# Optimization experiments

Measured on AMD Instinct MI355X. Metric: run time of the kernel, lower is better.

Reference implementation:

```python
import jax, jax.numpy as jnp
import numpy as np

E = 1024
M = 6
GH = 256
FR = 16  # FiLM bottleneck r = max(16, E//64)


def setup_inputs() -> dict:
    key = jax.random.key(0)
    ks = jax.random.split(key, 32)
    n = lambda k, shape, std=0.02: jax.random.normal(k, shape, dtype=jnp.float32) * std
    inp = {
        "x": jax.random.normal(ks[0], (4, 2048, E), dtype=jnp.float32),
        # gate MLP E->GH->M
        "gw1": n(ks[1], (E, GH)), "gb1": jnp.zeros((GH,), jnp.float32),
        "gw2": n(ks[2], (GH, M)), "gb2": jnp.zeros((M,), jnp.float32),
        "ebias": jnp.zeros((M,), jnp.float32),
        "pm_alpha": jnp.float32(0.5),
        # expert 0: DoubleMLP E->2E->E
        "dfc_w": n(ks[3], (E, 2 * E)), "dfc_b": jnp.zeros((2 * E,), jnp.float32),
        "dproj_w": n(ks[4], (2 * E, E)), "dproj_b": jnp.zeros((E,), jnp.float32),
        # expert 1: SingleMLP E->E->E
        "sfc_w": n(ks[5], (E, E)), "sfc_b": jnp.zeros((E,), jnp.float32),
        "sproj_w": n(ks[6], (E, E)), "sproj_b": jnp.zeros((E,), jnp.float32),
        # expert 2: rank-2 perceptron
        "p2_w": n(ks[7], (2, E)), "p2_v": n(ks[8], (2, E)),
        "p2_alpha": jnp.ones((2,), jnp.float32), "p2_b": jnp.zeros((2,), jnp.float32),
        "p2_bias": jnp.zeros((E,), jnp.float32),
        # expert 3: rank-4 perceptron
        "p4_w": n(ks[9], (4, E)), "p4_v": n(ks[10], (4, E)),
        "p4_alpha": jnp.ones((4,), jnp.float32), "p4_b": jnp.zeros((4,), jnp.float32),
        "p4_bias": jnp.zeros((E,), jnp.float32),
        # expert 4: ReGLU1D
        "rg_u": n(ks[11], (E,)), "rg_a": jnp.ones((E,), jnp.float32),
        "rg_b": jnp.zeros((1,), jnp.float32), "rg_bias": jnp.zeros((E,), jnp.float32),
        # expert 5: FiLM E->FR->2E
        "fl_dw": n(ks[12], (E, FR)), "fl_db": jnp.zeros((FR,), jnp.float32),
        "fl_uw": n(ks[13], (FR, 2 * E)), "fl_ub": jnp.zeros((2 * E,), jnp.float32),
    }
    return inp


def _gelu(x):
    return jax.nn.gelu(x, approximate=False)  # torch nn.GELU default (erf)


def _rank_n(x, w, v, alpha, b, biasvec):
    # y = biasvec + sum_i alpha_i * gelu(<w_i,x> + b_i) * v_i
    s = jnp.einsum("bse,ne->bsn", x, w) + b
    g = _gelu(s)
    return jnp.einsum("bsn,ne->bse", alpha * g, v) + biasvec


def reference(x, gw1, gb1, gw2, gb2, ebias, pm_alpha,
              dfc_w, dfc_b, dproj_w, dproj_b,
              sfc_w, sfc_b, sproj_w, sproj_b,
              p2_w, p2_v, p2_alpha, p2_b, p2_bias,
              p4_w, p4_v, p4_alpha, p4_b, p4_bias,
              rg_u, rg_a, rg_b, rg_bias,
              fl_dw, fl_db, fl_uw, fl_ub):
    # gate logits [B,S,M]; tau=1.0
    gl = _gelu(x @ gw1 + gb1) @ gw2 + gb2 + ebias
    pi = jax.nn.softmax(gl, axis=-1)
    # top_k=1 sparse weights: mask to top-1 then renormalize
    _, topi = jax.lax.top_k(pi, 1)
    mask = jax.nn.one_hot(topi[..., 0], M, dtype=pi.dtype)
    w = pi * mask
    w = w / (jnp.sum(w, axis=-1, keepdims=True) + 1e-9)

    # experts (dropout = identity in eval)
    o0 = _gelu(x @ dfc_w + dfc_b) @ dproj_w + dproj_b            # DoubleMLP
    o1 = _gelu(x @ sfc_w + sfc_b) @ sproj_w + sproj_b            # SingleMLP
    o2 = _rank_n(x, p2_w, p2_v, p2_alpha, p2_b, p2_bias)          # perc2
    o3 = _rank_n(x, p4_w, p4_v, p4_alpha, p4_b, p4_bias)          # perc4
    s = x @ rg_u + rg_b[0]                                        # ReGLU1D
    o4 = jax.nn.sigmoid(s)[..., None] * (x * rg_a) + rg_bias
    t = _gelu(x @ fl_dw + fl_db)                                  # FiLM
    gb = t @ fl_uw + fl_ub
    gamma, beta = jnp.split(gb, 2, axis=-1)
    o5 = gamma * x + beta

    all_out = jnp.stack([o0, o1, o2, o3, o4, o5], axis=-1)        # [B,S,E,M]
    mixed = jnp.sum(all_out * w[..., None, :], axis=-1)
    return pm_alpha * mixed
```

## Files before the change

### kernel.cpp

```cpp
#include <hip/hip_runtime.h>
#include <math.h>


#define E 1024
#define GH 256
#define NEXP 6
#define NTOK 8192
#define NCH 24

typedef __attribute__((ext_vector_type(8))) short bf16x8;
typedef __attribute__((ext_vector_type(4))) float f32x4;

__device__ __forceinline__ float gelu_erf(float v) {
    return 0.5f * v * (1.0f + erff(v * 0.70710678118654752440f));
}

__device__ __forceinline__ unsigned short f2bf(float f) {
    union { float f; unsigned u; } c; c.f = f;
    unsigned u = c.u;
    u += 0x7fffu + ((u >> 16) & 1u);
    return (unsigned short)(u >> 16);
}

__device__ __forceinline__ float bf2f(unsigned short h) {
    union { unsigned u; float f; } c; c.u = ((unsigned)h) << 16;
    return c.f;
}

__device__ __forceinline__ int ldso(int row, int q) {
    return row * 32 + ((q ^ ((row >> 1) & 3)) << 3);
}

__global__ __launch_bounds__(256)
void prep_kernel(const float* __restrict__ x, unsigned short* __restrict__ xh,
                 unsigned short* __restrict__ xl,
                 const float* __restrict__ gw1, unsigned short* __restrict__ w1cat,
                 const float* __restrict__ p2_w, const float* __restrict__ p4_w,
                 const float* __restrict__ rg_u, const float* __restrict__ fl_dw,
                 unsigned short* __restrict__ w1cheap,
                 const float* __restrict__ dfc_w, unsigned short* __restrict__ dfc_wt,
                 const float* __restrict__ dproj_w, unsigned short* __restrict__ dpj_wt,
                 const float* __restrict__ sfc_w, unsigned short* __restrict__ sfc_wt,
                 const float* __restrict__ sproj_w, unsigned short* __restrict__ spj_wt) {
    __shared__ float tile[32][33];
    const int tid = threadIdx.x;
    const int tx = tid & 31, ty = tid >> 5;
    int b = blockIdx.x;
    if (b < 2048) {
        const int n4 = NTOK * E / 4;
        for (int i = b * 256 + tid; i < n4; i += 2048 * 256) {
            float4 v = reinterpret_cast<const float4*>(x)[i];
            ushort4 h, l;
            h.x = f2bf(v.x); l.x = f2bf(v.x - bf2f(h.x));
            h.y = f2bf(v.y); l.y = f2bf(v.y - bf2f(h.y));
            h.z = f2bf(v.z); l.z = f2bf(v.z - bf2f(h.z));
            h.w = f2bf(v.w); l.w = f2bf(v.w - bf2f(h.w));
            reinterpret_cast<ushort4*>(xh)[i] = h;
            reinterpret_cast<ushort4*>(xl)[i] = l;
        }
        return;
    }
    b -= 2048;
    if (b < 256) {
        const int c0 = (b & 7) * 32, r0 = (b >> 3) * 32;
#pragma unroll
        for (int i = 0; i < 4; ++i)
            tile[ty + i * 8][tx] = gw1[(size_t)(r0 + ty + i * 8) * GH + c0 + tx];
        __syncthreads();
#pragma unroll
        for (int i = 0; i < 4; ++i) {
            float v = tile[tx][ty + i * 8];
            unsigned short h = f2bf(v);
            size_t row = (size_t)(c0 + ty + i * 8) * 2048;
            w1cat[row + r0 + tx] = h;
            w1cat[row + 1024 + r0 + tx] = f2bf(v - bf2f(h));
        }
        return;
    }
    b -= 256;
    if (b < 64) {
        const int r = b;
        const int k4 = tid * 4;
        float4 v = {0.f, 0.f, 0.f, 0.f};
        if (r < 2)       v = *reinterpret_cast<const float4*>(&p2_w[r * E + k4]);
        else if (r < 6)  v = *reinterpret_cast<const float4*>(&p4_w[(r - 2) * E + k4]);
        else if (r == 6) v = *reinterpret_cast<const float4*>(&rg_u[k4]);
        else if (r < 23) {
            const int j = r - 7;
            v.x = fl_dw[(k4 + 0) * 16 + j];
            v.y = fl_dw[(k4 + 1) * 16 + j];
            v.z = fl_dw[(k4 + 2) * 16 + j];
            v.w = fl_dw[(k4 + 3) * 16 + j];
        }
        ushort4 h, l;
        h.x = f2bf(v.x); l.x = f2bf(v.x - bf2f(h.x));
        h.y = f2bf(v.y); l.y = f2bf(v.y - bf2f(h.y));
        h.z = f2bf(v.z); l.z = f2bf(v.z - bf2f(h.z));
        h.w = f2bf(v.w); l.w = f2bf(v.w - bf2f(h.w));
        *reinterpret_cast<ushort4*>(&w1cheap[r * 2048 + k4]) = h;
        *reinterpret_cast<ushort4*>(&w1cheap[r * 2048 + 1024 + k4]) = l;
        return;
    }
    b -= 64;
    const float* src; unsigned short* dst; int R, C, nbx;
    if (b < 2048)      { src = dfc_w;   dst = dfc_wt; R = 1024; C = 2048; nbx = 64; }
    else if (b < 4096) { src = dproj_w; dst = dpj_wt; R = 2048; C = 1024; nbx = 32; b -= 2048; }
    else if (b < 5120) { src = sfc_w;   dst = sfc_wt; R = 1024; C = 1024; nbx = 32; b -= 4096; }
    else               { src = sproj_w; dst = spj_wt; R = 1024; C = 1024; nbx = 32; b -= 5120; }
    const int c0 = (b % nbx) * 32, r0 = (b / nbx) * 32;
#pragma unroll
    for (int i = 0; i < 4; ++i)
        tile[ty + i * 8][tx] = src[(size_t)(r0 + ty + i * 8) * C + c0 + tx];
    __syncthreads();
#pragma unroll
    for (int i = 0; i < 4; ++i)
        dst[(size_t)(c0 + ty + i * 8) * R + r0 + tx] = f2bf(tile[tx][ty + i * 8]);
}

__global__ __launch_bounds__(256)
void gate_partial_kernel(const unsigned short* __restrict__ xh,
                         const unsigned short* __restrict__ xl,
                         const unsigned short* __restrict__ w1cat,
                         const unsigned short* __restrict__ w1cheap,
                         float* __restrict__ hp0, float* __restrict__ hp1,
                         float* __restrict__ cdot0, float* __restrict__ cdot1) {
    __shared__ __align__(16) unsigned short As[2][64 * 32];
    __shared__ __align__(16) unsigned short Bs[2][64 * 32];
    const int tid = threadIdx.x;
    const int t0 = blockIdx.y * 64, n0 = blockIdx.x * 64, z = blockIdx.z;
    const unsigned short* A = z ? xl : xh;
    float* hp = z ? hp1 : hp0;
    float* cd = z ? cdot1 : cdot0;

    const int lane = tid & 63, wv = tid >> 6;
    const int wm = (wv & 1) * 32, wn = (wv >> 1) * 32;
    const int lm = lane & 15, q = lane >> 4;
    const int r0 = tid >> 2, gsl = tid & 3;
    const int g = gsl ^ ((r0 >> 1) & 3);
    const int so = r0 * 32 + gsl * 8;

    const unsigned short* pa = A + (size_t)(t0 + r0) * E + g * 8;
    const unsigned short* pb = w1cat + (size_t)(n0 + r0) * 2048 + g * 8;

    const bool docheap = (blockIdx.x == 0);
    const int tc = wv >> 1;
    const unsigned short* pcw = w1cheap + (size_t)(tc * 16 + lm) * 2048 + q * 8;

    f32x4 acc[2][2];
#pragma unroll
    for (int s = 0; s < 2; ++s)
#pragma unroll
        for (int t = 0; t < 2; ++t) acc[s][t] = (f32x4){0.f, 0.f, 0.f, 0.f};
    f32x4 accC[2];
    accC[0] = (f32x4){0.f, 0.f, 0.f, 0.f};
    accC[1] = (f32x4){0.f, 0.f, 0.f, 0.f};

    bf16x8 ra = *(const bf16x8*)(pa);
    bf16x8 rb = *(const bf16x8*)(pb);
    bf16x8 cfv, cfn;
    if (docheap) cfv = *(const bf16x8*)(pcw);
    *(bf16x8*)&As[0][so] = ra;
    *(bf16x8*)&Bs[0][so] = rb;

    int cur = 0, k0 = 0;
    while (true) {
        __syncthreads();
        const int kn = k0 + 32;
        if (kn < 2048) {
            ra = *(const bf16x8*)(pa + (kn & 1023));
            rb = *(const bf16x8*)(pb + kn);
            if (docheap) cfn = *(const bf16x8*)(pcw + kn);
        }
        bf16x8 af[2], bf[2];
#pragma unroll
        for (int s = 0; s < 2; ++s) af[s] = *(const bf16x8*)&As[cur][ldso(wm + s * 16 + lm, q)];
#pragma unroll
        for (int t = 0; t < 2; ++t) bf[t] = *(const bf16x8*)&Bs[cur][ldso(wn + t * 16 + lm, q)];
#pragma unroll
        for (int s = 0; s < 2; ++s)
#pragma unroll
            for (int t = 0; t < 2; ++t)
                acc[s][t] = __builtin_amdgcn_mfma_f32_16x16x32_bf16(af[s], bf[t], acc[s][t], 0, 0, 0);
        if (docheap) {
            accC[0] = __builtin_amdgcn_mfma_f32_16x16x32_bf16(af[0], cfv, accC[0], 0, 0, 0);
            accC[1] = __builtin_amdgcn_mfma_f32_16x16x32_bf16(af[1], cfv, accC[1], 0, 0, 0);
        }
        if (kn >= 2048) break;
        *(bf16x8*)&As[cur ^ 1][so] = ra;
        *(bf16x8*)&Bs[cur ^ 1][so] = rb;
        cfv = cfn;
        cur ^= 1; k0 = kn;
    }
#pragma unroll
    for (int s = 0; s < 2; ++s)
#pragma unroll
        for (int t = 0; t < 2; ++t)
#pragma unroll
            for (int rg = 0; rg < 4; ++rg) {
                int rl = wm + s * 16 + q * 4 + rg;
                int c  = wn + t * 16 + lm;
                hp[(size_t)(t0 + rl) * GH + n0 + c] = acc[s][t][rg];
            }
    if (docheap) {
        const int c = tc * 16 + lm;
        if (c < NCH) {
#pragma unroll
            for (int s = 0; s < 2; ++s)
#pragma unroll
                for (int rg = 0; rg < 4; ++rg) {
                    int rl = wm + s * 16 + q * 4 + rg;
                    cd[(size_t)(t0 + rl) * NCH + c] = accC[s][rg];
                }
        }
    }
}

__global__ __launch_bounds__(256)
void gate_finalize_kernel(const float* __restrict__ hp0, const float* __restrict__ hp1,
                          const float* __restrict__ gb1, const float* __restrict__ gw2,
                          const float* __restrict__ gb2, const float* __restrict__ ebias,
                          const float* __restrict__ pm_alpha,
                          const float* __restrict__ cdot0, const float* __restrict__ cdot1,
                          const float* __restrict__ p2_alpha, const float* __restrict__ p2_b,
                          const float* __restrict__ p4_alpha, const float* __restrict__ p4_b,
                          const float* __restrict__ rg_b, const float* __restrict__ fl_db,
                          float* __restrict__ scale, int* __restrict__ counts,
                          int* __restrict__ tlist, int* __restrict__ eid,
                          float* __restrict__ gvec) {
    __shared__ float hs[32][264];
    __shared__ float g2s[GH * NEXP];
    __shared__ int tokexp[32];
    const int tid = threadIdx.x;
    const int t0 = blockIdx.x * 32;
    for (int i = tid; i < GH * NEXP; i += 256) g2s[i] = gw2[i];
#pragma unroll
    for (int i = 0; i < 8; ++i) {
        int f4 = i * 256 + tid;
        int row = f4 >> 6, c4 = (f4 & 63) * 4;
        size_t base = (size_t)(t0 + row) * GH + c4;
        float4 a = *reinterpret_cast<const float4*>(&hp0[base]);
        float4 b = *reinterpret_cast<const float4*>(&hp1[base]);
        float4 o;
        o.x = gelu_erf(a.x + b.x + gb1[c4 + 0]);
        o.y = gelu_erf(a.y + b.y + gb1[c4 + 1]);
        o.z = gelu_erf(a.z + b.z + gb1[c4 + 2]);
        o.w = gelu_erf(a.w + b.w + gb1[c4 + 3]);
        *reinterpret_cast<float4*>(&hs[row][c4]) = o;
    }
    __syncthreads();
    const int t = tid >> 3, j = tid & 7;
    float p[NEXP] = {0.f, 0.f, 0.f, 0.f, 0.f, 0.f};
#pragma unroll 8
    for (int kk = 0; kk < 32; ++kk) {
        int k = j + kk * 8;
        float hv = hs[t][k];
        const float* gr = &g2s[k * NEXP];
#pragma unroll
        for (int m = 0; m < NEXP; ++m) p[m] += hv * gr[m];
    }
#pragma unroll
    for (int m = 0; m < NEXP; ++m) {
        p[m] += __shfl_xor(p[m], 4, 64);
        p[m] += __shfl_xor(p[m], 2, 64);
        p[m] += __shfl_xor(p[m], 1, 64);
    }
    if (j == 0) {
        float L[NEXP];
#pragma unroll
        for (int m = 0; m < NEXP; ++m) L[m] = p[m] + gb2[m] + ebias[m];
        float mx = L[0]; int am = 0;
#pragma unroll
        for (int m = 1; m < NEXP; ++m) { if (L[m] > mx) { mx = L[m]; am = m; } }
        float S = 0.f;
#pragma unroll
        for (int m = 0; m < NEXP; ++m) S += expf(L[m] - mx);
        float pt = 1.f / S;
        scale[t0 + t] = pm_alpha[0] * (pt / (pt + 1e-9f));
        eid[t0 + t] = am;
        tokexp[t] = am;
    }
    __syncthreads();
    if (tid < NEXP) {
        const int e = tid;
        int cnt = 0;
#pragma unroll
        for (int i = 0; i < 32; ++i) cnt += (tokexp[i] == e);
        if (cnt) {
            int base = atomicAdd(&counts[e], cnt);
            int pos = 0;
#pragma unroll
            for (int i = 0; i < 32; ++i)
                if (tokexp[i] == e) tlist[e * NTOK + base + (pos++)] = t0 + i;
        }
    }
    for (int i = tid; i < 32 * NCH; i += 256) {
        const int tt = i / NCH, slot = i - tt * NCH;
        const int tok = t0 + tt;
        float s = cdot0[(size_t)tok * NCH + slot] + cdot1[(size_t)tok * NCH + slot];
        float val;
        if (slot < 2)       val = p2_alpha[slot] * gelu_erf(s + p2_b[slot]);
        else if (slot < 6)  val = p4_alpha[slot - 2] * gelu_erf(s + p4_b[slot - 2]);
        else if (slot == 6) val = 1.f / (1.f + expf(-(s + rg_b[0])));
        else if (slot < 23) val = gelu_erf(s + fl_db[slot - 7]);
        else                val = 0.f;
        gvec[(size_t)tok * NCH + slot] = val;
    }
}

__global__ __launch_bounds__(256)
void moe_gemm1_kernel(const unsigned short* __restrict__ xh,
                      const unsigned short* __restrict__ B0, const unsigned short* __restrict__ B1,
                      const float* __restrict__ bias0, const float* __restrict__ bias1,
                      const int* __restrict__ counts, const int* __restrict__ tlist,
                      unsigned short* __restrict__ H0, unsigned short* __restrict__ H1) {
    const int z = blockIdx.z;
    const int N = z ? 1024 : 2048;
    const int cnt = counts[z];
    const int i0 = blockIdx.y * 64;
    const int n0 = blockIdx.x * 64;
    if (i0 >= cnt || n0 >= N) return;
    const unsigned short* Bz = z ? B1 : B0;
    const float* bias = z ? bias1 : bias0;

    __shared__ __align__(16) unsigned short As[2][64 * 32];
    __shared__ __align__(16) unsigned short Bs[2][64 * 32];
    __shared__ int toks[64];
    const int tid = threadIdx.x;
    if (tid < 64) toks[tid] = tlist[z * NTOK + min(i0 + tid, cnt - 1)];
    __syncthreads();

    const int lane = tid & 63, wv = tid >> 6;
    const int wm = (wv & 1) * 32, wn = (wv >> 1) * 32;
    const int lm = lane & 15, q = lane >> 4;
    const int r0 = tid >> 2, gsl = tid & 3;
    const int g = gsl ^ ((r0 >> 1) & 3);
    const int so = r0 * 32 + gsl * 8;

    const unsigned short* pa = xh + (size_t)toks[r0] * E + g * 8;
    const unsigned short* pb = Bz + (size_t)(n0 + r0) * E + g * 8;

    f32x4 acc[2][2];
#pragma unroll
    for (int s = 0; s < 2; ++s)
#pragma unroll
        for (int t = 0; t < 2; ++t) acc[s][t] = (f32x4){0.f, 0.f, 0.f, 0.f};

    bf16x8 ra = *(const bf16x8*)(pa);
    bf16x8 rb = *(const bf16x8*)(pb);
    *(bf16x8*)&As[0][so] = ra;
    *(bf16x8*)&Bs[0][so] = rb;

    int cur = 0, k0 = 0;
    while (true) {
        __syncthreads();
        const int kn = k0 + 32;
        if (kn < E) {
            ra = *(const bf16x8*)(pa + kn);
            rb = *(const bf16x8*)(pb + kn);
        }
        bf16x8 af[2], bf[2];
#pragma unroll
        for (int s = 0; s < 2; ++s) af[s] = *(const bf16x8*)&As[cur][ldso(wm + s * 16 + lm, q)];
#pragma unroll
        for (int t = 0; t < 2; ++t) bf[t] = *(const bf16x8*)&Bs[cur][ldso(wn + t * 16 + lm, q)];
#pragma unroll
        for (int s = 0; s < 2; ++s)
#pragma unroll
            for (int t = 0; t < 2; ++t)
                acc[s][t] = __builtin_amdgcn_mfma_f32_16x16x32_bf16(af[s], bf[t], acc[s][t], 0, 0, 0);
        if (kn >= E) break;
        *(bf16x8*)&As[cur ^ 1][so] = ra;
        *(bf16x8*)&Bs[cur ^ 1][so] = rb;
        cur ^= 1; k0 = kn;
    }
    unsigned short* Hz = z ? H1 : H0;
#pragma unroll
    for (int s = 0; s < 2; ++s)
#pragma unroll
        for (int t = 0; t < 2; ++t)
#pragma unroll
            for (int rg = 0; rg < 4; ++rg) {
                int rl = wm + s * 16 + q * 4 + rg;
                int gc = n0 + wn + t * 16 + lm;
                float v = acc[s][t][rg] + bias[gc];
                Hz[(size_t)(i0 + rl) * N + gc] = f2bf(gelu_erf(v));
            }
}

__global__ __launch_bounds__(256)
void gemm2_cheap_kernel(const unsigned short* __restrict__ h1, const unsigned short* __restrict__ h2,
                        const unsigned short* __restrict__ dpj, const unsigned short* __restrict__ spj,
                        const float* __restrict__ dproj_b, const float* __restrict__ sproj_b,
                        const int* __restrict__ counts, const int* __restrict__ tlist,
                        const float* __restrict__ scale,
                        const float* __restrict__ x, const int* __restrict__ eid,
                        const float* __restrict__ gvec,
                        const float* __restrict__ p2_v, const float* __restrict__ p2_bias,
                        const float* __restrict__ p4_v, const float* __restrict__ p4_bias,
                        const float* __restrict__ rg_a, const float* __restrict__ rg_bias,
                        const float* __restrict__ fl_uw, const float* __restrict__ fl_ub,
                        float* __restrict__ out) {
    __shared__ __align__(16) char smem[2 * 64 * 32 * 2 * 2 + 64 * 4];
    const int tid = threadIdx.x;
    const int bb = blockIdx.x;
    const int lane = tid & 63;

    if (bb < 1024) {
        const int z = bb >> 9;
        const int r = bb & 511;
        const int n0 = (r & 15) * 64;
        const int i0 = (r >> 4) * 64;
        const int K = z ? 1024 : 2048;
        const int cnt = counts[z];
        if (i0 >= cnt) return;
        const int rows = min(64, cnt - i0);
        const unsigned short* Az = z ? h2 : h1;
        const unsigned short* Bz = z ? spj : dpj;
        const float* bias = z ? sproj_b : dproj_b;

        unsigned short (*As)[64 * 32] = (unsigned short (*)[64 * 32])smem;
        unsigned short (*Bs)[64 * 32] = (unsigned short (*)[64 * 32])(smem + 2 * 64 * 32 * 2);
        int* toks = (int*)(smem + 2 * 64 * 32 * 2 * 2);
        if (tid < 64) toks[tid] = tlist[z * NTOK + min(i0 + tid, cnt - 1)];
        __syncthreads();

        const int wv = tid >> 6;
        const int wm = (wv & 1) * 32, wn = (wv >> 1) * 32;
        const int lm = lane & 15, q = lane >> 4;
        const int r0 = tid >> 2, gsl = tid & 3;
        const int g = gsl ^ ((r0 >> 1) & 3);
        const int so = r0 * 32 + gsl * 8;

        const unsigned short* pa = Az + (size_t)(i0 + r0) * K + g * 8;
        const unsigned short* pb = Bz + (size_t)(n0 + r0) * K + g * 8;

        f32x4 acc[2][2];
#pragma unroll
        for (int s = 0; s < 2; ++s)
#pragma unroll
            for (int t = 0; t < 2; ++t) acc[s][t] = (f32x4){0.f, 0.f, 0.f, 0.f};

        bf16x8 ra = *(const bf16x8*)(pa);
        bf16x8 rb = *(const bf16x8*)(pb);
        *(bf16x8*)&As[0][so] = ra;
        *(bf16x8*)&Bs[0][so] = rb;

        int cur = 0, k0 = 0;
        while (true) {
            __syncthreads();
            const int kn = k0 + 32;
            if (kn < K) {
                ra = *(const bf16x8*)(pa + kn);
                rb = *(const bf16x8*)(pb + kn);
            }
            bf16x8 af[2], bf[2];
#pragma unroll
            for (int s = 0; s < 2; ++s) af[s] = *(const bf16x8*)&As[cur][ldso(wm + s * 16 + lm, q)];
#pragma unroll
            for (int t = 0; t < 2; ++t) bf[t] = *(const bf16x8*)&Bs[cur][ldso(wn + t * 16 + lm, q)];
#pragma unroll
            for (int s = 0; s < 2; ++s)
#pragma unroll
                for (int t = 0; t < 2; ++t)
                    acc[s][t] = __builtin_amdgcn_mfma_f32_16x16x32_bf16(af[s], bf[t], acc[s][t], 0, 0, 0);
            if (kn >= K) break;
            *(bf16x8*)&As[cur ^ 1][so] = ra;
            *(bf16x8*)&Bs[cur ^ 1][so] = rb;
            cur ^= 1; k0 = kn;
        }
#pragma unroll
        for (int s = 0; s < 2; ++s)
#pragma unroll
            for (int t = 0; t < 2; ++t)
#pragma unroll
                for (int rg = 0; rg < 4; ++rg) {
                    int rl = wm + s * 16 + q * 4 + rg;
                    if (rl < rows) {
                        int gc = n0 + wn + t * 16 + lm;
                        int tok = toks[rl];
                        out[(size_t)tok * E + gc] = scale[tok] * (acc[s][t][rg] + bias[gc]);
                    }
                }
        return;
    }

    const int tok = bb - 1024;
    const int e = eid[tok];
    if (e < 2) return;
    const float sc = scale[tok];
    const int k4 = tid * 4;
    const float* gv = &gvec[(size_t)tok * NCH];
    float4 o;

    if (e == 2) {
        const float g0 = gv[0], g1 = gv[1];
        float4 b0 = *reinterpret_cast<const float4*>(&p2_bias[k4]);
        float4 v0 = *reinterpret_cast<const float4*>(&p2_v[k4]);
        float4 v1 = *reinterpret_cast<const float4*>(&p2_v[E + k4]);
        o.x = b0.x + g0 * v0.x + g1 * v1.x;
        o.y = b0.y + g0 * v0.y + g1 * v1.y;
        o.z = b0.z + g0 * v0.z + g1 * v1.z;
        o.w = b0.w + g0 * v0.w + g1 * v1.w;
    } else if (e == 3) {
        o = *reinterpret_cast<const float4*>(&p4_bias[k4]);
#pragma unroll
        for (int j = 0; j < 4; ++j) {
            const float gj = gv[2 + j];
            float4 vv = *reinterpret_cast<const float4*>(&p4_v[j * E + k4]);
            o.x += gj * vv.x; o.y += gj * vv.y; o.z += gj * vv.z; o.w += gj * vv.w;
        }
    } else if (e == 4) {
        const float sg = gv[6];
        float4 xv = *reinterpret_cast<const float4*>(&x[(size_t)tok * E + k4]);
        float4 av = *reinterpret_cast<const float4*>(&rg_a[k4]);
        float4 bv = *reinterpret_cast<const float4*>(&rg_bias[k4]);
        o.x = sg * xv.x * av.x + bv.x;
        o.y = sg * xv.y * av.y + bv.y;
        o.z = sg * xv.z * av.z + bv.z;
        o.w = sg * xv.w * av.w + bv.w;
    } else {
        float4 xv = *reinterpret_cast<const float4*>(&x[(size_t)tok * E + k4]);
        float4 ga = *reinterpret_cast<const float4*>(&fl_ub[k4]);
        float4 be = *reinterpret_cast<const float4*>(&fl_ub[E + k4]);
#pragma unroll
        for (int j = 0; j < 16; ++j) {
            const float tj = gv[7 + j];
            float4 ug = *reinterpret_cast<const float4*>(&fl_uw[(size_t)j * 2 * E + k4]);
            float4 ub = *reinterpret_cast<const float4*>(&fl_uw[(size_t)j * 2 * E + E + k4]);
            ga.x += tj * ug.x; ga.y += tj * ug.y; ga.z += tj * ug.z; ga.w += tj * ug.w;
            be.x += tj * ub.x; be.y += tj * ub.y; be.z += tj * ub.z; be.w += tj * ub.w;
        }
        o.x = ga.x * xv.x + be.x;
        o.y = ga.y * xv.y + be.y;
        o.z = ga.z * xv.z + be.z;
        o.w = ga.w * xv.w + be.w;
    }
    o.x *= sc; o.y *= sc; o.z *= sc; o.w *= sc;
    *reinterpret_cast<float4*>(&out[(size_t)tok * E + k4]) = o;
}

extern "C" void kernel_launch(void* const* d_in, const int* in_sizes, int n_in,
                              void* d_out, int out_size, void* d_ws, size_t ws_size,
                              hipStream_t stream) {
    const float* x        = (const float*)d_in[0];
    const float* gw1      = (const float*)d_in[1];
    const float* gb1      = (const float*)d_in[2];
    const float* gw2      = (const float*)d_in[3];
    const float* gb2      = (const float*)d_in[4];
    const float* ebias    = (const float*)d_in[5];
    const float* pm_alpha = (const float*)d_in[6];
    const float* dfc_w    = (const float*)d_in[7];
    const float* dfc_b    = (const float*)d_in[8];
    const float* dproj_w  = (const float*)d_in[9];
    const float* dproj_b  = (const float*)d_in[10];
    const float* sfc_w    = (const float*)d_in[11];
    const float* sfc_b    = (const float*)d_in[12];
    const float* sproj_w  = (const float*)d_in[13];
    const float* sproj_b  = (const float*)d_in[14];
    const float* p2_w     = (const float*)d_in[15];
    const float* p2_v     = (const float*)d_in[16];
    const float* p2_alpha = (const float*)d_in[17];
    const float* p2_b     = (const float*)d_in[18];
    const float* p2_bias  = (const float*)d_in[19];
    const float* p4_w     = (const float*)d_in[20];
    const float* p4_v     = (const float*)d_in[21];
    const float* p4_alpha = (const float*)d_in[22];
    const float* p4_b     = (const float*)d_in[23];
    const float* p4_bias  = (const float*)d_in[24];
    const float* rg_u     = (const float*)d_in[25];
    const float* rg_a     = (const float*)d_in[26];
    const float* rg_b     = (const float*)d_in[27];
    const float* rg_bias  = (const float*)d_in[28];
    const float* fl_dw    = (const float*)d_in[29];
    const float* fl_db    = (const float*)d_in[30];
    const float* fl_uw    = (const float*)d_in[31];
    const float* fl_ub    = (const float*)d_in[32];
    float* out = (float*)d_out;

    char* ws = (char*)d_ws;
    size_t off = 0;
    int*            counts = (int*)(ws + off);            off += 256;
    float*          scale  = (float*)(ws + off);          off += (size_t)NTOK * 4;
    int*            tlist  = (int*)(ws + off);            off += (size_t)NEXP * NTOK * 4;
    int*            eid    = (int*)(ws + off);            off += (size_t)NTOK * 4;
    float*          gvec   = (float*)(ws + off);          off += (size_t)NTOK * NCH * 4;
    unsigned short* w1cheap= (unsigned short*)(ws + off); off += (size_t)64 * 2048 * 2;
    unsigned short* w1cat  = (unsigned short*)(ws + off); off += (size_t)GH * 2048 * 2;
    unsigned short* dfc_wt = (unsigned short*)(ws + off); off += (size_t)2048 * 1024 * 2;
    unsigned short* dpj_wt = (unsigned short*)(ws + off); off += (size_t)1024 * 2048 * 2;
    unsigned short* sfc_wt = (unsigned short*)(ws + off); off += (size_t)1024 * 1024 * 2;
    unsigned short* spj_wt = (unsigned short*)(ws + off); off += (size_t)1024 * 1024 * 2;
    unsigned short* x_hi   = (unsigned short*)(ws + off); off += (size_t)NTOK * E * 2;
    char* U = ws + off;
    unsigned short* x_lo = (unsigned short*)U;
    float*          hp0  = (float*)(U + (size_t)16 * 1024 * 1024);
    float*          hp1  = (float*)(U + (size_t)24 * 1024 * 1024);
    unsigned short* h1   = (unsigned short*)U;
    unsigned short* h2   = (unsigned short*)(U + (size_t)16 * 1024 * 1024);
    float* cdot0 = out;
    float* cdot1 = out + (size_t)NTOK * NCH;

    hipMemsetAsync(counts, 0, 256, stream);
    prep_kernel<<<8512, 256, 0, stream>>>(x, x_hi, x_lo, gw1, w1cat,
                                          p2_w, p4_w, rg_u, fl_dw, w1cheap,
                                          dfc_w, dfc_wt, dproj_w, dpj_wt,
                                          sfc_w, sfc_wt, sproj_w, spj_wt);
    gate_partial_kernel<<<dim3(GH / 64, NTOK / 64, 2), 256, 0, stream>>>(
        x_hi, x_lo, w1cat, w1cheap, hp0, hp1, cdot0, cdot1);
    gate_finalize_kernel<<<NTOK / 32, 256, 0, stream>>>(
        hp0, hp1, gb1, gw2, gb2, ebias, pm_alpha, cdot0, cdot1,
        p2_alpha, p2_b, p4_alpha, p4_b, rg_b, fl_db,
        scale, counts, tlist, eid, gvec);
    moe_gemm1_kernel<<<dim3(32, 32, 2), 256, 0, stream>>>(
        x_hi, dfc_wt, sfc_wt, dfc_b, sfc_b, counts, tlist, h1, h2);
    gemm2_cheap_kernel<<<1024 + NTOK, 256, 0, stream>>>(
        h1, h2, dpj_wt, spj_wt, dproj_b, sproj_b, counts, tlist, scale,
        x, eid, gvec,
        p2_v, p2_bias, p4_v, p4_bias,
        rg_a, rg_bias, fl_uw, fl_ub, out);
    (void)in_sizes; (void)n_in; (void)out_size; (void)ws_size;
}
```

Baseline: 304.0 us.

## Use 128x128 tiles with direct global-to-LDS loads and XCD-aware block mapping

```diff
diff --git a/kernel.cpp b/kernel.cpp
--- a/kernel.cpp
+++ b/kernel.cpp
@@ -29,6 +29,12 @@
 
 __device__ __forceinline__ int ldso(int row, int q) {
     return row * 32 + ((q ^ ((row >> 1) & 3)) << 3);
+}
+
+__device__ __forceinline__ void glds16(const void* g, void* l) {
+    __builtin_amdgcn_global_load_lds(
+        (const __attribute__((address_space(1))) void*)g,
+        (__attribute__((address_space(3))) void*)l, 16, 0, 0);
 }
 
 __global__ __launch_bounds__(256)
@@ -122,105 +128,109 @@
                          const unsigned short* __restrict__ xl,
                          const unsigned short* __restrict__ w1cat,
                          const unsigned short* __restrict__ w1cheap,
-                         float* __restrict__ hp0, float* __restrict__ hp1,
-                         float* __restrict__ cdot0, float* __restrict__ cdot1) {
-    __shared__ __align__(16) unsigned short As[2][64 * 32];
-    __shared__ __align__(16) unsigned short Bs[2][64 * 32];
+                         float* __restrict__ hp,
+                         float* __restrict__ cdot) {
+    __shared__ __align__(16) unsigned short As[2][128 * 32];
+    __shared__ __align__(16) unsigned short Bs[2][128 * 32];
     const int tid = threadIdx.x;
-    const int t0 = blockIdx.y * 64, n0 = blockIdx.x * 64, z = blockIdx.z;
+    const int bid = blockIdx.x;
+    const int xcd = bid & 7, slot = bid >> 3;
+    const int nx = slot & 1;
+    const int strip = xcd * 32 + (slot >> 1);
+    const int m = strip >> 2, c2 = strip & 3;
+    const int z = c2 & 1, h = c2 >> 1;
+    const int t0 = m * 128, n0 = nx * 128;
     const unsigned short* A = z ? xl : xh;
-    float* hp = z ? hp1 : hp0;
-    float* cd = z ? cdot1 : cdot0;
+    float* hpz = hp + (size_t)c2 * ((size_t)NTOK * GH);
+    float* cd  = cdot + (size_t)c2 * ((size_t)NTOK * NCH);
 
     const int lane = tid & 63, wv = tid >> 6;
-    const int wm = (wv & 1) * 32, wn = (wv >> 1) * 32;
+    const int wr = wv >> 1, wc = wv & 1;
     const int lm = lane & 15, q = lane >> 4;
     const int r0 = tid >> 2, gsl = tid & 3;
     const int g = gsl ^ ((r0 >> 1) & 3);
-    const int so = r0 * 32 + gsl * 8;
-
-    const unsigned short* pa = A + (size_t)(t0 + r0) * E + g * 8;
-    const unsigned short* pb = w1cat + (size_t)(n0 + r0) * 2048 + g * 8;
-
-    const bool docheap = (blockIdx.x == 0);
-    const int tc = wv >> 1;
-    const unsigned short* pcw = w1cheap + (size_t)(tc * 16 + lm) * 2048 + q * 8;
-
-    f32x4 acc[2][2];
-#pragma unroll
-    for (int s = 0; s < 2; ++s)
-#pragma unroll
-        for (int t = 0; t < 2; ++t) acc[s][t] = (f32x4){0.f, 0.f, 0.f, 0.f};
+    const int lbase = wv * 512;
+
+    const unsigned short* pa0 = A + (size_t)(t0 + r0) * E + g * 8;
+    const unsigned short* pa1 = A + (size_t)(t0 + 64 + r0) * E + g * 8;
+    const unsigned short* pb0 = w1cat + (size_t)(n0 + r0) * 2048 + h * 1024 + g * 8;
+    const unsigned short* pb1 = w1cat + (size_t)(n0 + 64 + r0) * 2048 + h * 1024 + g * 8;
+    const unsigned short* pcw = w1cheap + (size_t)(nx * 16 + lm) * 2048 + h * 1024 + q * 8;
+
+    f32x4 acc[4][4];
+#pragma unroll
+    for (int s = 0; s < 4; ++s)
+#pragma unroll
+        for (int t = 0; t < 4; ++t) acc[s][t] = (f32x4){0.f, 0.f, 0.f, 0.f};
     f32x4 accC[2];
     accC[0] = (f32x4){0.f, 0.f, 0.f, 0.f};
     accC[1] = (f32x4){0.f, 0.f, 0.f, 0.f};
 
-    bf16x8 ra = *(const bf16x8*)(pa);
-    bf16x8 rb = *(const bf16x8*)(pb);
-    bf16x8 cfv, cfn;
-    if (docheap) cfv = *(const bf16x8*)(pcw);
-    *(bf16x8*)&As[0][so] = ra;
-    *(bf16x8*)&Bs[0][so] = rb;
-
-    int cur = 0, k0 = 0;
-    while (true) {
+    glds16(pa0, &As[0][lbase]);
+    glds16(pa1, &As[0][2048 + lbase]);
+    glds16(pb0, &Bs[0][lbase]);
+    glds16(pb1, &Bs[0][2048 + lbase]);
+    bf16x8 cfv = *(const bf16x8*)pcw;
+
+    int cur = 0;
+    for (int k0 = 0;; k0 += 32) {
         __syncthreads();
         const int kn = k0 + 32;
-        if (kn < 2048) {
-            ra = *(const bf16x8*)(pa + (kn & 1023));
-            rb = *(const bf16x8*)(pb + kn);
-            if (docheap) cfn = *(const bf16x8*)(pcw + kn);
-        }
-        bf16x8 af[2], bf[2];
-#pragma unroll
-        for (int s = 0; s < 2; ++s) af[s] = *(const bf16x8*)&As[cur][ldso(wm + s * 16 + lm, q)];
-#pragma unroll
-        for (int t = 0; t < 2; ++t) bf[t] = *(const bf16x8*)&Bs[cur][ldso(wn + t * 16 + lm, q)];
-#pragma unroll
-        for (int s = 0; s < 2; ++s)
-#pragma unroll
-            for (int t = 0; t < 2; ++t)
-                acc[s][t] = __builtin_amdgcn_mfma_f32_16x16x32_bf16(af[s], bf[t], acc[s][t], 0, 0, 0);
-        if (docheap) {
-            accC[0] = __builtin_amdgcn_mfma_f32_16x16x32_bf16(af[0], cfv, accC[0], 0, 0, 0);
-            accC[1] = __builtin_amdgcn_mfma_f32_16x16x32_bf16(af[1], cfv, accC[1], 0, 0, 0);
-        }
-        if (kn >= 2048) break;
-        *(bf16x8*)&As[cur ^ 1][so] = ra;
-        *(bf16x8*)&Bs[cur ^ 1][so] = rb;
-        cfv = cfn;
-        cur ^= 1; k0 = kn;
-    }
-#pragma unroll
-    for (int s = 0; s < 2; ++s)
-#pragma unroll
-        for (int t = 0; t < 2; ++t)
+        bf16x8 cfn;
+        if (kn < 1024) {
+            glds16(pa0 + kn, &As[cur ^ 1][lbase]);
+            glds16(pa1 + kn, &As[cur ^ 1][2048 + lbase]);
+            glds16(pb0 + kn, &Bs[cur ^ 1][lbase]);
+            glds16(pb1 + kn, &Bs[cur ^ 1][2048 + lbase]);
+            cfn = *(const bf16x8*)(pcw + kn);
+        }
+        bf16x8 af[4], bfr[4];
+#pragma unroll
+        for (int s = 0; s < 4; ++s) af[s] = *(const bf16x8*)&As[cur][ldso(wr * 64 + s * 16 + lm, q)];
+#pragma unroll
+        for (int t = 0; t < 4; ++t) bfr[t] = *(const bf16x8*)&Bs[cur][ldso(wc * 64 + t * 16 + lm, q)];
+#pragma unroll
+        for (int s = 0; s < 4; ++s)
+#pragma unroll
+            for (int t = 0; t < 4; ++t)
+                acc[s][t] = __builtin_amdgcn_mfma_f32_16x16x32_bf16(af[s], bfr[t], acc[s][t], 0, 0, 0);
+        {
+            bf16x8 ac0 = wc ? af[2] : af[0];
+            bf16x8 ac1 = wc ? af[3] : af[1];
+            accC[0] = __builtin_amdgcn_mfma_f32_16x16x32_bf16(ac0, cfv, accC[0], 0, 0, 0);
+            accC[1] = __builtin_amdgcn_mfma_f32_16x16x32_bf16(ac1, cfv, accC[1], 0, 0, 0);
+        }
+        if (kn >= 1024) break;
+        cfv = cfn; cur ^= 1;
+    }
+#pragma unroll
+    for (int s = 0; s < 4; ++s)
+#pragma unroll
+        for (int t = 0; t < 4; ++t)
 #pragma unroll
             for (int rg = 0; rg < 4; ++rg) {
-                int rl = wm + s * 16 + q * 4 + rg;
-                int c  = wn + t * 16 + lm;
-                hp[(size_t)(t0 + rl) * GH + n0 + c] = acc[s][t][rg];
+                int rl = wr * 64 + s * 16 + q * 4 + rg;
+                int c  = wc * 64 + t * 16 + lm;
+                hpz[(size_t)(t0 + rl) * GH + n0 + c] = acc[s][t][rg];
             }
-    if (docheap) {
-        const int c = tc * 16 + lm;
-        if (c < NCH) {
-#pragma unroll
-            for (int s = 0; s < 2; ++s)
-#pragma unroll
-                for (int rg = 0; rg < 4; ++rg) {
-                    int rl = wm + s * 16 + q * 4 + rg;
-                    cd[(size_t)(t0 + rl) * NCH + c] = accC[s][rg];
-                }
-        }
+    const int cc = nx * 16 + lm;
+    if (cc < NCH) {
+#pragma unroll
+        for (int i = 0; i < 2; ++i)
+#pragma unroll
+            for (int rg = 0; rg < 4; ++rg) {
+                int rl = wr * 64 + wc * 32 + i * 16 + q * 4 + rg;
+                cd[(size_t)(t0 + rl) * NCH + cc] = accC[i][rg];
+            }
     }
 }
 
 __global__ __launch_bounds__(256)
-void gate_finalize_kernel(const float* __restrict__ hp0, const float* __restrict__ hp1,
+void gate_finalize_kernel(const float* __restrict__ hp,
                           const float* __restrict__ gb1, const float* __restrict__ gw2,
                           const float* __restrict__ gb2, const float* __restrict__ ebias,
                           const float* __restrict__ pm_alpha,
-                          const float* __restrict__ cdot0, const float* __restrict__ cdot1,
+                          const float* __restrict__ cdot,
                           const float* __restrict__ p2_alpha, const float* __restrict__ p2_b,
                           const float* __restrict__ p4_alpha, const float* __restrict__ p4_b,
                           const float* __restrict__ rg_b, const float* __restrict__ fl_db,
@@ -232,19 +242,22 @@
     __shared__ int tokexp[32];
     const int tid = threadIdx.x;
     const int t0 = blockIdx.x * 32;
+    const size_t HPS = (size_t)NTOK * GH;
     for (int i = tid; i < GH * NEXP; i += 256) g2s[i] = gw2[i];
 #pragma unroll
     for (int i = 0; i < 8; ++i) {
         int f4 = i * 256 + tid;
         int row = f4 >> 6, c4 = (f4 & 63) * 4;
         size_t base = (size_t)(t0 + row) * GH + c4;
-        float4 a = *reinterpret_cast<const float4*>(&hp0[base]);
-        float4 b = *reinterpret_cast<const float4*>(&hp1[base]);
+        float4 a = *reinterpret_cast<const float4*>(&hp[base]);
+        float4 b = *reinterpret_cast<const float4*>(&hp[HPS + base]);
+        float4 c = *reinterpret_cast<const float4*>(&hp[2 * HPS + base]);
+        float4 d = *reinterpret_cast<const float4*>(&hp[3 * HPS + base]);
         float4 o;
-        o.x = gelu_erf(a.x + b.x + gb1[c4 + 0]);
-        o.y = gelu_erf(a.y + b.y + gb1[c4 + 1]);
-        o.z = gelu_erf(a.z + b.z + gb1[c4 + 2]);
-        o.w = gelu_erf(a.w + b.w + gb1[c4 + 3]);
+        o.x = gelu_erf(a.x + b.x + c.x + d.x + gb1[c4 + 0]);
+        o.y = gelu_erf(a.y + b.y + c.y + d.y + gb1[c4 + 1]);
+        o.z = gelu_erf(a.z + b.z + c.z + d.z + gb1[c4 + 2]);
+        o.w = gelu_erf(a.w + b.w + c.w + d.w + gb1[c4 + 3]);
         *reinterpret_cast<float4*>(&hs[row][c4]) = o;
     }
     __syncthreads();
@@ -293,10 +306,12 @@
                 if (tokexp[i] == e) tlist[e * NTOK + base + (pos++)] = t0 + i;
         }
     }
+    const size_t CDS = (size_t)NTOK * NCH;
     for (int i = tid; i < 32 * NCH; i += 256) {
         const int tt = i / NCH, slot = i - tt * NCH;
         const int tok = t0 + tt;
-        float s = cdot0[(size_t)tok * NCH + slot] + cdot1[(size_t)tok * NCH + slot];
+        size_t idx = (size_t)tok * NCH + slot;
+        float s = cdot[idx] + cdot[CDS + idx] + cdot[2 * CDS + idx] + cdot[3 * CDS + idx];
         float val;
         if (slot < 2)       val = p2_alpha[slot] * gelu_erf(s + p2_b[slot]);
         else if (slot < 6)  val = p4_alpha[slot - 2] * gelu_erf(s + p4_b[slot - 2]);
@@ -313,75 +328,81 @@
                       const float* __restrict__ bias0, const float* __restrict__ bias1,
                       const int* __restrict__ counts, const int* __restrict__ tlist,
                       unsigned short* __restrict__ H0, unsigned short* __restrict__ H1) {
-    const int z = blockIdx.z;
+    __shared__ __align__(16) unsigned short As[2][128 * 32];
+    __shared__ __align__(16) unsigned short Bs[2][128 * 32];
+    __shared__ int toks[128];
+    const int tid = threadIdx.x;
+    const int bid = blockIdx.x;
+    const int xcd = bid & 7, slot = bid >> 3;
+    int z, l, nx;
+    if (slot < 32) { z = 0; l = slot >> 4; nx = slot & 15; }
+    else           { z = 1; l = (slot - 32) >> 3; nx = (slot - 32) & 7; }
+    const int mtile = xcd + 8 * l;
+    const int i0 = mtile * 128, n0 = nx * 128;
     const int N = z ? 1024 : 2048;
     const int cnt = counts[z];
-    const int i0 = blockIdx.y * 64;
-    const int n0 = blockIdx.x * 64;
-    if (i0 >= cnt || n0 >= N) return;
+    if (i0 >= cnt) return;
     const unsigned short* Bz = z ? B1 : B0;
     const float* bias = z ? bias1 : bias0;
 
-    __shared__ __align__(16) unsigned short As[2][64 * 32];
-    __shared__ __align__(16) unsigned short Bs[2][64 * 32];
-    __shared__ int toks[64];
-    const int tid = threadIdx.x;
-    if (tid < 64) toks[tid] = tlist[z * NTOK + min(i0 + tid, cnt - 1)];
+    if (tid < 128) toks[tid] = tlist[z * NTOK + min(i0 + tid, cnt - 1)];
     __syncthreads();
 
     const int lane = tid & 63, wv = tid >> 6;
-    const int wm = (wv & 1) * 32, wn = (wv >> 1) * 32;
+    const int wr = wv >> 1, wc = wv & 1;
     const int lm = lane & 15, q = lane >> 4;
     const int r0 = tid >> 2, gsl = tid & 3;
     const int g = gsl ^ ((r0 >> 1) & 3);
-    const int so = r0 * 32 + gsl * 8;
-
-    const unsigned short* pa = xh + (size_t)toks[r0] * E + g * 8;
-    const unsigned short* pb = Bz + (size_t)(n0 + r0) * E + g * 8;
-
-    f32x4 acc[2][2];
-#pragma unroll
-    for (int s = 0; s < 2; ++s)
-#pragma unroll
-        for (int t = 0; t < 2; ++t) acc[s][t] = (f32x4){0.f, 0.f, 0.f, 0.f};
-
-    bf16x8 ra = *(const bf16x8*)(pa);
-    bf16x8 rb = *(const bf16x8*)(pb);
-    *(bf16x8*)&As[0][so] = ra;
-    *(bf16x8*)&Bs[0][so] = rb;
-
-    int cur = 0, k0 = 0;
-    while (true) {
+    const int lbase = wv * 512;
+
+    const unsigned short* pa0 = xh + (size_t)toks[r0] * E + g * 8;
+    const unsigned short* pa1 = xh + (size_t)toks[64 + r0] * E + g * 8;
+    const unsigned short* pb0 = Bz + (size_t)(n0 + r0) * E + g * 8;
+    const unsigned short* pb1 = Bz + (size_t)(n0 + 64 + r0) * E + g * 8;
+
+    f32x4 acc[4][4];
+#pragma unroll
+    for (int s = 0; s < 4; ++s)
+#pragma unroll
+        for (int t = 0; t < 4; ++t) acc[s][t] = (f32x4){0.f, 0.f, 0.f, 0.f};
+
+    glds16(pa0, &As[0][lbase]);
+    glds16(pa1, &As[0][2048 + lbase]);
+    glds16(pb0, &Bs[0][lbase]);
+    glds16(pb1, &Bs[0][2048 + lbase]);
+
+    int cur = 0;
+    for (int k0 = 0;; k0 += 32) {
         __syncthreads();
         const int kn = k0 + 32;
         if (kn < E) {
-            ra = *(const bf16x8*)(pa + kn);
-            rb = *(const bf16x8*)(pb + kn);
-        }
-        bf16x8 af[2], bf[2];
-#pragma unroll
-        for (int s = 0; s < 2; ++s) af[s] = *(const bf16x8*)&As[cur][ldso(wm + s * 16 + lm, q)];
-#pragma unroll
-        for (int t = 0; t < 2; ++t) bf[t] = *(const bf16x8*)&Bs[cur][ldso(wn + t * 16 + lm, q)];
-#pragma unroll
-        for (int s = 0; s < 2; ++s)
-#pragma unroll
-            for (int t = 0; t < 2; ++t)
-                acc[s][t] = __builtin_amdgcn_mfma_f32_16x16x32_bf16(af[s], bf[t], acc[s][t], 0, 0, 0);
+            glds16(pa0 + kn, &As[cur ^ 1][lbase]);
+            glds16(pa1 + kn, &As[cur ^ 1][2048 + lbase]);
+            glds16(pb0 + kn, &Bs[cur ^ 1][lbase]);
+            glds16(pb1 + kn, &Bs[cur ^ 1][2048 + lbase]);
+        }
+        bf16x8 af[4], bfr[4];
+#pragma unroll
+        for (int s = 0; s < 4; ++s) af[s] = *(const bf16x8*)&As[cur][ldso(wr * 64 + s * 16 + lm, q)];
+#pragma unroll
+        for (int t = 0; t < 4; ++t) bfr[t] = *(const bf16x8*)&Bs[cur][ldso(wc * 64 + t * 16 + lm, q)];
+#pragma unroll
+        for (int s = 0; s < 4; ++s)
+#pragma unroll
+            for (int t = 0; t < 4; ++t)
+                acc[s][t] = __builtin_amdgcn_mfma_f32_16x16x32_bf16(af[s], bfr[t], acc[s][t], 0, 0, 0);
         if (kn >= E) break;
-        *(bf16x8*)&As[cur ^ 1][so] = ra;
-        *(bf16x8*)&Bs[cur ^ 1][so] = rb;
-        cur ^= 1; k0 = kn;
+        cur ^= 1;
     }
     unsigned short* Hz = z ? H1 : H0;
 #pragma unroll
-    for (int s = 0; s < 2; ++s)
-#pragma unroll
-        for (int t = 0; t < 2; ++t)
+    for (int s = 0; s < 4; ++s)
+#pragma unroll
+        for (int t = 0; t < 4; ++t)
 #pragma unroll
             for (int rg = 0; rg < 4; ++rg) {
-                int rl = wm + s * 16 + q * 4 + rg;
-                int gc = n0 + wn + t * 16 + lm;
+                int rl = wr * 64 + s * 16 + q * 4 + rg;
+                int gc = n0 + wc * 64 + t * 16 + lm;
                 float v = acc[s][t][rg] + bias[gc];
                 Hz[(size_t)(i0 + rl) * N + gc] = f2bf(gelu_erf(v));
             }
@@ -400,83 +421,86 @@
                         const float* __restrict__ rg_a, const float* __restrict__ rg_bias,
                         const float* __restrict__ fl_uw, const float* __restrict__ fl_ub,
                         float* __restrict__ out) {
-    __shared__ __align__(16) char smem[2 * 64 * 32 * 2 * 2 + 64 * 4];
+    __shared__ __align__(16) unsigned short As[2][128 * 32];
+    __shared__ __align__(16) unsigned short Bs[2][128 * 32];
+    __shared__ int toks[128];
     const int tid = threadIdx.x;
     const int bb = blockIdx.x;
     const int lane = tid & 63;
 
-    if (bb < 1024) {
-        const int z = bb >> 9;
-        const int r = bb & 511;
-        const int n0 = (r & 15) * 64;
-        const int i0 = (r >> 4) * 64;
+    if (bb < 256) {
+        const int xcd = bb & 7, slot = bb >> 3;
+        const int z = slot >> 4;
+        const int s2 = slot & 15;
+        const int l = s2 >> 3, nx = s2 & 7;
+        const int mtile = xcd + 8 * l;
+        const int i0 = mtile * 128, n0 = nx * 128;
         const int K = z ? 1024 : 2048;
         const int cnt = counts[z];
         if (i0 >= cnt) return;
-        const int rows = min(64, cnt - i0);
+        const int rows = min(128, cnt - i0);
         const unsigned short* Az = z ? h2 : h1;
         const unsigned short* Bz = z ? spj : dpj;
         const float* bias = z ? sproj_b : dproj_b;
 
-        unsigned short (*As)[64 * 32] = (unsigned short (*)[64 * 32])smem;
-        unsigned short (*Bs)[64 * 32] = (unsigned short (*)[64 * 32])(smem + 2 * 64 * 32 * 2);
-        int* toks = (int*)(smem + 2 * 64 * 32 * 2 * 2);
-        if (tid < 64) toks[tid] = tlist[z * NTOK + min(i0 + tid, cnt - 1)];
+        if (tid < 128) toks[tid] = tlist[z * NTOK + min(i0 + tid, cnt - 1)];
         __syncthreads();
 
         const int wv = tid >> 6;
-        const int wm = (wv & 1) * 32, wn = (wv >> 1) * 32;
+        const int wr = wv >> 1, wc = wv & 1;
         const int lm = lane & 15, q = lane >> 4;
         const int r0 = tid >> 2, gsl = tid & 3;
         const int g = gsl ^ ((r0 >> 1) & 3);
-        const int so = r0 * 32 + gsl * 8;
-
-        const unsigned short* pa = Az + (size_t)(i0 + r0) * K + g * 8;
-        const unsigned short* pb = Bz + (size_t)(n0 + r0) * K + g * 8;
-
-        f32x4 acc[2][2];
-#pragma unroll
-        for (int s = 0; s < 2; ++s)
-#pragma unroll
-            for (int t = 0; t < 2; ++t) acc[s][t] = (f32x4){0.f, 0.f, 0.f, 0.f};
-
-        bf16x8 ra = *(const bf16x8*)(pa);
-        bf16x8 rb = *(const bf16x8*)(pb);
-        *(bf16x8*)&As[0][so] = ra;
-        *(bf16x8*)&Bs[0][so] = rb;
-
-        int cur = 0, k0 = 0;
-        while (true) {
+        const int lbase = wv * 512;
+
+        const unsigned short* pa0 = Az + (size_t)(i0 + r0) * K + g * 8;
+        const unsigned short* pa1 = Az + (size_t)(i0 + 64 + r0) * K + g * 8;
+        const unsigned short* pb0 = Bz + (size_t)(n0 + r0) * K + g * 8;
+        const unsigned short* pb1 = Bz + (size_t)(n0 + 64 + r0) * K + g * 8;
+
+        f32x4 acc[4][4];
+#pragma unroll
+        for (int s = 0; s < 4; ++s)
+#pragma unroll
+            for (int t = 0; t < 4; ++t) acc[s][t] = (f32x4){0.f, 0.f, 0.f, 0.f};
+
+        glds16(pa0, &As[0][lbase]);
+        glds16(pa1, &As[0][2048 + lbase]);
+        glds16(pb0, &Bs[0][lbase]);
+        glds16(pb1, &Bs[0][2048 + lbase]);
+
+        int cur = 0;
+        for (int k0 = 0;; k0 += 32) {
             __syncthreads();
             const int kn = k0 + 32;
             if (kn < K) {
-                ra = *(const bf16x8*)(pa + kn);
-                rb = *(const bf16x8*)(pb + kn);
+                glds16(pa0 + kn, &As[cur ^ 1][lbase]);
+                glds16(pa1 + kn, &As[cur ^ 1][2048 + lbase]);
+                glds16(pb0 + kn, &Bs[cur ^ 1][lbase]);
+                glds16(pb1 + kn, &Bs[cur ^ 1][2048 + lbase]);
             }
-            bf16x8 af[2], bf[2];
-#pragma unroll
-            for (int s = 0; s < 2; ++s) af[s] = *(const bf16x8*)&As[cur][ldso(wm + s * 16 + lm, q)];
-#pragma unroll
-            for (int t = 0; t < 2; ++t) bf[t] = *(const bf16x8*)&Bs[cur][ldso(wn + t * 16 + lm, q)];
-#pragma unroll
-            for (int s = 0; s < 2; ++s)
-#pragma unroll
-                for (int t = 0; t < 2; ++t)
-                    acc[s][t] = __builtin_amdgcn_mfma_f32_16x16x32_bf16(af[s], bf[t], acc[s][t], 0, 0, 0);
+            bf16x8 af[4], bfr[4];
+#pragma unroll
+            for (int s = 0; s < 4; ++s) af[s] = *(const bf16x8*)&As[cur][ldso(wr * 64 + s * 16 + lm, q)];
+#pragma unroll
+            for (int t = 0; t < 4; ++t) bfr[t] = *(const bf16x8*)&Bs[cur][ldso(wc * 64 + t * 16 + lm, q)];
+#pragma unroll
+            for (int s = 0; s < 4; ++s)
+#pragma unroll
+                for (int t = 0; t < 4; ++t)
+                    acc[s][t] = __builtin_amdgcn_mfma_f32_16x16x32_bf16(af[s], bfr[t], acc[s][t], 0, 0, 0);
             if (kn >= K) break;
-            *(bf16x8*)&As[cur ^ 1][so] = ra;
-            *(bf16x8*)&Bs[cur ^ 1][so] = rb;
-            cur ^= 1; k0 = kn;
-        }
-#pragma unroll
-        for (int s = 0; s < 2; ++s)
-#pragma unroll
-            for (int t = 0; t < 2; ++t)
+            cur ^= 1;
+        }
+#pragma unroll
+        for (int s = 0; s < 4; ++s)
+#pragma unroll
+            for (int t = 0; t < 4; ++t)
 #pragma unroll
                 for (int rg = 0; rg < 4; ++rg) {
-                    int rl = wm + s * 16 + q * 4 + rg;
+                    int rl = wr * 64 + s * 16 + q * 4 + rg;
                     if (rl < rows) {
-                        int gc = n0 + wn + t * 16 + lm;
+                        int gc = n0 + wc * 64 + t * 16 + lm;
                         int tok = toks[rl];
                         out[(size_t)tok * E + gc] = scale[tok] * (acc[s][t][rg] + bias[gc]);
                     }
@@ -484,7 +508,7 @@
         return;
     }
 
-    const int tok = bb - 1024;
+    const int tok = bb - 256;
     const int e = eid[tok];
     if (e < 2) return;
     const float sc = scale[tok];
@@ -584,6 +608,7 @@
     int*            tlist  = (int*)(ws + off);            off += (size_t)NEXP * NTOK * 4;
     int*            eid    = (int*)(ws + off);            off += (size_t)NTOK * 4;
     float*          gvec   = (float*)(ws + off);          off += (size_t)NTOK * NCH * 4;
+    float*          cdot   = (float*)(ws + off);          off += (size_t)4 * NTOK * NCH * 4;
     unsigned short* w1cheap= (unsigned short*)(ws + off); off += (size_t)64 * 2048 * 2;
     unsigned short* w1cat  = (unsigned short*)(ws + off); off += (size_t)GH * 2048 * 2;
     unsigned short* dfc_wt = (unsigned short*)(ws + off); off += (size_t)2048 * 1024 * 2;
@@ -593,27 +618,24 @@
     unsigned short* x_hi   = (unsigned short*)(ws + off); off += (size_t)NTOK * E * 2;
     char* U = ws + off;
     unsigned short* x_lo = (unsigned short*)U;
-    float*          hp0  = (float*)(U + (size_t)16 * 1024 * 1024);
-    float*          hp1  = (float*)(U + (size_t)24 * 1024 * 1024);
     unsigned short* h1   = (unsigned short*)U;
     unsigned short* h2   = (unsigned short*)(U + (size_t)16 * 1024 * 1024);
-    float* cdot0 = out;
-    float* cdot1 = out + (size_t)NTOK * NCH;
+    float* hp = out;
 
     hipMemsetAsync(counts, 0, 256, stream);
     prep_kernel<<<8512, 256, 0, stream>>>(x, x_hi, x_lo, gw1, w1cat,
                                           p2_w, p4_w, rg_u, fl_dw, w1cheap,
                                           dfc_w, dfc_wt, dproj_w, dpj_wt,
                                           sfc_w, sfc_wt, sproj_w, spj_wt);
-    gate_partial_kernel<<<dim3(GH / 64, NTOK / 64, 2), 256, 0, stream>>>(
-        x_hi, x_lo, w1cat, w1cheap, hp0, hp1, cdot0, cdot1);
+    gate_partial_kernel<<<512, 256, 0, stream>>>(
+        x_hi, x_lo, w1cat, w1cheap, hp, cdot);
     gate_finalize_kernel<<<NTOK / 32, 256, 0, stream>>>(
-        hp0, hp1, gb1, gw2, gb2, ebias, pm_alpha, cdot0, cdot1,
+        hp, gb1, gw2, gb2, ebias, pm_alpha, cdot,
         p2_alpha, p2_b, p4_alpha, p4_b, rg_b, fl_db,
         scale, counts, tlist, eid, gvec);
-    moe_gemm1_kernel<<<dim3(32, 32, 2), 256, 0, stream>>>(
+    moe_gemm1_kernel<<<384, 256, 0, stream>>>(
         x_hi, dfc_wt, sfc_wt, dfc_b, sfc_b, counts, tlist, h1, h2);
-    gemm2_cheap_kernel<<<1024 + NTOK, 256, 0, stream>>>(
+    gemm2_cheap_kernel<<<256 + NTOK, 256, 0, stream>>>(
         h1, h2, dpj_wt, spj_wt, dproj_b, sproj_b, counts, tlist, scale,
         x, eid, gvec,
         p2_v, p2_bias, p4_v, p4_bias,
```

Result: no change. 305.6 us (+0.5%).
